# Performance work log

Measured on AMD Instinct MI355X. Metric: run time of the kernel, lower is better.

The kernel has to match this reference:

```python
import jax, jax.numpy as jnp
import numpy as np

N_NODES = 100000
N_EDGES = 640000
LATDIM = 128
GNN_LAYER = 3
LN_EPS = 1e-5


def setup_inputs() -> dict:
    key = jax.random.key(0)
    k1, k2, k3, k4 = jax.random.split(key, 4)
    embeds = jax.random.normal(k1, (N_NODES, LATDIM), dtype=jnp.float32)
    adj_row = jax.random.randint(k2, (N_EDGES,), 0, N_NODES, dtype=jnp.int32)
    adj_col = jax.random.randint(k3, (N_EDGES,), 0, N_NODES, dtype=jnp.int32)
    adj_val = jax.random.uniform(k4, (N_EDGES,), dtype=jnp.float32)
    return {"embeds": embeds, "adj_row": adj_row, "adj_col": adj_col, "adj_val": adj_val}


def _layer_norm(x):
    # nn.LayerNorm(latdim, elementwise_affine=False)
    mu = jnp.mean(x, axis=-1, keepdims=True)
    var = jnp.mean(jnp.square(x - mu), axis=-1, keepdims=True)
    return (x - mu) / jnp.sqrt(var + LN_EPS)


def _spmm(adj_row, adj_col, adj_val, x):
    # out[r] += val * x[c] for each edge (r, c, val)  -- sparse [N,N] @ [N,d]
    msgs = adj_val[:, None] * x[adj_col]  # [E, d]
    return jax.ops.segment_sum(msgs, adj_row, num_segments=N_NODES)


def reference(embeds, adj_row, adj_col, adj_val):
    x = _layer_norm(embeds)
    acc = jnp.zeros_like(x)  # gnn_layer > 0, so hop-0 embeds are NOT included
    for _ in range(GNN_LAYER):
        x = _spmm(adj_row, adj_col, adj_val, x)
        acc = acc + x
    return acc
```

## Files before the change

kernel.cpp:

```cpp
#include <hip/hip_runtime.h>

#define N_NODES 100000
#define N_EDGES 640000
#define LATDIM  128
#define LN_EPS  1e-5f

typedef unsigned int u32;
typedef float f32x4 __attribute__((ext_vector_type(4)));

#define SCAN_NB   98
#define N_PAD     (SCAN_NB * 1024)

#define LN_BLOCKS   (N_NODES / 8)
#define HIST_BLOCKS ((N_EDGES + 255) / 256)

__device__ __forceinline__ float bflo(u32 u) { return __uint_as_float(u << 16); }
__device__ __forceinline__ float bfhi(u32 u) { return __uint_as_float(u & 0xffff0000u); }
__device__ __forceinline__ u32 pack_bf2(float a, float b) {
    u32 ua = __float_as_uint(a), ub = __float_as_uint(b);
    ua = (ua + 0x7fffu + ((ua >> 16) & 1u)) >> 16;
    ub = (ub + 0x7fffu + ((ub >> 16) & 1u)) >> 16;
    return ua | (ub << 16);
}

__device__ __forceinline__ u32 pack_edge(int col, float val) {
    u32 q = (u32)fminf(val * 32768.0f + 0.5f, 32767.0f);
    return (u32)col | (q << 17);
}
__device__ __forceinline__ int   edge_col(u32 r) { return (int)(r & 0x1FFFFu); }
__device__ __forceinline__ float edge_val(u32 r) { return (float)(r >> 17) * (1.0f / 32768.0f); }

__global__ __launch_bounds__(256) void ln_hist_kernel(const float* __restrict__ in,
                                                      u32* __restrict__ out,
                                                      const int* __restrict__ rowi,
                                                      int* __restrict__ cnt) {
    int b = blockIdx.x;
    if (b < LN_BLOCKS) {
        int tid  = threadIdx.x;
        int wave = tid >> 6;
        int lane = tid & 63;
        int half = lane >> 5;
        int sub  = lane & 31;
        int row  = b * 8 + wave * 2 + half;
        f32x4 v = __builtin_nontemporal_load(((const f32x4*)in) + (size_t)row * 32 + sub);
        float s  = v.x + v.y + v.z + v.w;
        float ss = v.x * v.x + v.y * v.y + v.z * v.z + v.w * v.w;
        #pragma unroll
        for (int o = 16; o > 0; o >>= 1) {
            s  += __shfl_xor(s,  o, 64);
            ss += __shfl_xor(ss, o, 64);
        }
        float mu   = s * (1.0f / LATDIM);
        float var  = ss * (1.0f / LATDIM) - mu * mu;
        float rstd = rsqrtf(var + LN_EPS);
        uint2 w;
        w.x = pack_bf2((v.x - mu) * rstd, (v.y - mu) * rstd);
        w.y = pack_bf2((v.z - mu) * rstd, (v.w - mu) * rstd);
        ((uint2*)out)[(size_t)row * 32 + sub] = w;
    } else {
        int e = (b - LN_BLOCKS) * 256 + threadIdx.x;
        if (e < N_EDGES) atomicAdd(&cnt[rowi[e]], 1);
    }
}

__global__ __launch_bounds__(256) void scan_ab_kernel(int* __restrict__ cnt,
                                                      int* __restrict__ bsums,
                                                      int* __restrict__ done) {
    __shared__ int ts[256];
    __shared__ int amLast;
    int t = threadIdx.x;
    int base = blockIdx.x * 1024 + t * 4;
    int4 v = *(const int4*)(cnt + base);
    int s = v.x + v.y + v.z + v.w;
    ts[t] = s;
    __syncthreads();
    #pragma unroll
    for (int o = 1; o < 256; o <<= 1) {
        int u = 0;
        if (t >= o) u = ts[t - o];
        __syncthreads();
        if (t >= o) ts[t] += u;
        __syncthreads();
    }
    int excl = ts[t] - s;
    int4 w;
    w.x = excl;
    w.y = excl + v.x;
    w.z = excl + v.x + v.y;
    w.w = excl + v.x + v.y + v.z;
    *(int4*)(cnt + base) = w;
    if (t == 255) {
        __hip_atomic_store(&bsums[blockIdx.x], ts[255],
                           __ATOMIC_RELEASE, __HIP_MEMORY_SCOPE_AGENT);
        int prev = __hip_atomic_fetch_add(done, 1,
                                          __ATOMIC_ACQ_REL, __HIP_MEMORY_SCOPE_AGENT);
        amLast = (prev == SCAN_NB - 1);
    }
    __syncthreads();
    if (amLast) {
        __shared__ int ss[128];
        int own = 0;
        if (t < 128) {
            own = (t < SCAN_NB)
                ? __hip_atomic_load(&bsums[t], __ATOMIC_ACQUIRE, __HIP_MEMORY_SCOPE_AGENT)
                : 0;
            ss[t] = own;
        }
        __syncthreads();
        #pragma unroll
        for (int o = 1; o < 128; o <<= 1) {
            int u = 0;
            if (t >= o && t < 128) u = ss[t - o];
            __syncthreads();
            if (t >= o && t < 128) ss[t] += u;
            __syncthreads();
        }
        if (t < SCAN_NB) bsums[t] = ss[t] - own;
    }
}

__global__ __launch_bounds__(256) void scatter_kernel(const int* __restrict__ rowi,
                                                      const int* __restrict__ coli,
                                                      const float* __restrict__ vali,
                                                      int* __restrict__ cursor,
                                                      const int* __restrict__ bsums,
                                                      u32* __restrict__ recs) {
    int e = blockIdx.x * 256 + threadIdx.x;
    if (e >= N_EDGES) return;
    int r = rowi[e];
    int pos = atomicAdd(&cursor[r], 1) + bsums[r >> 10];
    recs[pos] = pack_edge(coli[e], vali[e]);
}

__global__ __launch_bounds__(256) void spmm_csr_kernel(const int* __restrict__ row_end,
                                                       const int* __restrict__ bsums,
                                                       const u32* __restrict__ recs,
                                                       const u32* __restrict__ x,
                                                       u32* __restrict__ y,
                                                       const u32* __restrict__ add0,
                                                       const u32* __restrict__ add1,
                                                       float* __restrict__ out,
                                                       int mode) {
    int tid  = threadIdx.x;
    int wave = tid >> 6;
    int lane = tid & 63;
    int row  = blockIdx.x * 16 + wave * 4 + (lane >> 4);
    int sub  = lane & 15;
    int end = row_end[row] + bsums[row >> 10];
    int e   = row ? row_end[row - 1] + bsums[(row - 1) >> 10] : 0;
    const uint4* x4 = (const uint4*)x;
    float a0=0,a1=0,a2=0,a3=0,a4=0,a5=0,a6=0,a7=0;
    for (; e + 4 <= end; e += 4) {
        u32 r0 = recs[e], r1 = recs[e+1], r2 = recs[e+2], r3 = recs[e+3];
        uint4 g0 = x4[(size_t)edge_col(r0) * 16 + sub];
        uint4 g1 = x4[(size_t)edge_col(r1) * 16 + sub];
        uint4 g2 = x4[(size_t)edge_col(r2) * 16 + sub];
        uint4 g3 = x4[(size_t)edge_col(r3) * 16 + sub];
        float v0 = edge_val(r0), v1 = edge_val(r1);
        float v2 = edge_val(r2), v3 = edge_val(r3);
        a0 += v0 * bflo(g0.x); a1 += v0 * bfhi(g0.x);
        a2 += v0 * bflo(g0.y); a3 += v0 * bfhi(g0.y);
        a4 += v0 * bflo(g0.z); a5 += v0 * bfhi(g0.z);
        a6 += v0 * bflo(g0.w); a7 += v0 * bfhi(g0.w);
        a0 += v1 * bflo(g1.x); a1 += v1 * bfhi(g1.x);
        a2 += v1 * bflo(g1.y); a3 += v1 * bfhi(g1.y);
        a4 += v1 * bflo(g1.z); a5 += v1 * bfhi(g1.z);
        a6 += v1 * bflo(g1.w); a7 += v1 * bfhi(g1.w);
        a0 += v2 * bflo(g2.x); a1 += v2 * bfhi(g2.x);
        a2 += v2 * bflo(g2.y); a3 += v2 * bfhi(g2.y);
        a4 += v2 * bflo(g2.z); a5 += v2 * bfhi(g2.z);
        a6 += v2 * bflo(g2.w); a7 += v2 * bfhi(g2.w);
        a0 += v3 * bflo(g3.x); a1 += v3 * bfhi(g3.x);
        a2 += v3 * bflo(g3.y); a3 += v3 * bfhi(g3.y);
        a4 += v3 * bflo(g3.z); a5 += v3 * bfhi(g3.z);
        a6 += v3 * bflo(g3.w); a7 += v3 * bfhi(g3.w);
    }
    for (; e < end; ++e) {
        u32 r = recs[e];
        uint4 g = x4[(size_t)edge_col(r) * 16 + sub];
        float v = edge_val(r);
        a0 += v * bflo(g.x); a1 += v * bfhi(g.x);
        a2 += v * bflo(g.y); a3 += v * bfhi(g.y);
        a4 += v * bflo(g.z); a5 += v * bfhi(g.z);
        a6 += v * bflo(g.w); a7 += v * bfhi(g.w);
    }
    size_t oi = (size_t)row * 16 + sub;
    if (mode == 2) {
        uint4 b0 = ((const uint4*)add0)[oi];
        uint4 b1 = ((const uint4*)add1)[oi];
        a0 += bflo(b0.x) + bflo(b1.x); a1 += bfhi(b0.x) + bfhi(b1.x);
        a2 += bflo(b0.y) + bflo(b1.y); a3 += bfhi(b0.y) + bfhi(b1.y);
        a4 += bflo(b0.z) + bflo(b1.z); a5 += bfhi(b0.z) + bfhi(b1.z);
        a6 += bflo(b0.w) + bflo(b1.w); a7 += bfhi(b0.w) + bfhi(b1.w);
        f32x4* o4 = (f32x4*)(out + (size_t)row * LATDIM + sub * 8);
        f32x4 q0 = {a0, a1, a2, a3};
        f32x4 q1 = {a4, a5, a6, a7};
        __builtin_nontemporal_store(q0, o4 + 0);
        __builtin_nontemporal_store(q1, o4 + 1);
    } else {
        uint4 w;
        w.x = pack_bf2(a0, a1);
        w.y = pack_bf2(a2, a3);
        w.z = pack_bf2(a4, a5);
        w.w = pack_bf2(a6, a7);
        ((uint4*)y)[oi] = w;
    }
}

__global__ __launch_bounds__(256) void ln_f32_kernel(const float* __restrict__ in,
                                                     float* __restrict__ out) {
    int tid  = threadIdx.x;
    int wave = tid >> 6;
    int lane = tid & 63;
    int half = lane >> 5;
    int sub  = lane & 31;
    int row  = blockIdx.x * 8 + wave * 2 + half;
    if (row >= N_NODES) return;
    float4 v = ((const float4*)in)[(size_t)row * 32 + sub];
    float s  = v.x + v.y + v.z + v.w;
    float ss = v.x * v.x + v.y * v.y + v.z * v.z + v.w * v.w;
    #pragma unroll
    for (int o = 16; o > 0; o >>= 1) {
        s  += __shfl_xor(s,  o, 64);
        ss += __shfl_xor(ss, o, 64);
    }
    float mu   = s * (1.0f / LATDIM);
    float var  = ss * (1.0f / LATDIM) - mu * mu;
    float rstd = rsqrtf(var + LN_EPS);
    float4 o4;
    o4.x = (v.x - mu) * rstd; o4.y = (v.y - mu) * rstd;
    o4.z = (v.z - mu) * rstd; o4.w = (v.w - mu) * rstd;
    ((float4*)out)[(size_t)row * 32 + sub] = o4;
}

__global__ __launch_bounds__(256) void spmm_atomic_kernel(const int* __restrict__ rowi,
                                                          const int* __restrict__ coli,
                                                          const float* __restrict__ vali,
                                                          const float* __restrict__ x,
                                                          float* __restrict__ y) {
    int t = blockIdx.x * 256 + threadIdx.x;
    int e = t >> 5;
    if (e >= N_EDGES) return;
    int k = t & 31;
    int r = rowi[e];
    int c = coli[e];
    float v = vali[e];
    float4 xv = ((const float4*)(x + (size_t)c * LATDIM))[k];
    float* yp = y + (size_t)r * LATDIM + k * 4;
    atomicAdd(yp + 0, v * xv.x);
    atomicAdd(yp + 1, v * xv.y);
    atomicAdd(yp + 2, v * xv.z);
    atomicAdd(yp + 3, v * xv.w);
}

__global__ __launch_bounds__(256) void addz_kernel(float* __restrict__ acc,
                                                   const float* __restrict__ x,
                                                   float* __restrict__ z,
                                                   int first) {
    size_t i = (size_t)blockIdx.x * 256 + threadIdx.x;
    float4 xv = ((const float4*)x)[i];
    float4* ap = ((float4*)acc) + i;
    if (first) {
        *ap = xv;
    } else {
        float4 a = *ap;
        a.x += xv.x; a.y += xv.y; a.z += xv.z; a.w += xv.w;
        *ap = a;
    }
    if (z) ((float4*)z)[i] = make_float4(0.f, 0.f, 0.f, 0.f);
}

extern "C" void kernel_launch(void* const* d_in, const int* in_sizes, int n_in,
                              void* d_out, int out_size, void* d_ws, size_t ws_size,
                              hipStream_t stream) {
    const float* embeds  = (const float*)d_in[0];
    const int*   adj_row = (const int*)d_in[1];
    const int*   adj_col = (const int*)d_in[2];
    const float* adj_val = (const float*)d_in[3];
    float* out = (float*)d_out;

    u32*  A16  = (u32*)d_ws;
    u32*  B16  = A16 + (size_t)N_NODES * (LATDIM / 2);
    int*  cnt   = (int*)(B16 + (size_t)N_NODES * (LATDIM / 2));
    int*  bsums = cnt + N_PAD;
    int*  done  = bsums + 128;
    u32*  recs  = (u32*)(done + 32);
    size_t need = (size_t)((char*)(recs + N_EDGES) - (char*)d_ws);

    const int edgeGrid = (N_EDGES + 255) / 256;
    const int rowGrid  = N_NODES / 16;

    if (ws_size >= need) {
        hipMemsetAsync(cnt, 0, (size_t)(N_PAD + 128 + 32) * sizeof(int), stream);
        ln_hist_kernel<<<LN_BLOCKS + HIST_BLOCKS, 256, 0, stream>>>(embeds, A16,
                                                                    adj_row, cnt);
        scan_ab_kernel<<<SCAN_NB, 256, 0, stream>>>(cnt, bsums, done);
        scatter_kernel<<<edgeGrid, 256, 0, stream>>>(adj_row, adj_col, adj_val,
                                                     cnt, bsums, recs);
        spmm_csr_kernel<<<rowGrid, 256, 0, stream>>>(cnt, bsums, recs, A16, B16,
                                                     nullptr, nullptr, nullptr, 0);
        spmm_csr_kernel<<<rowGrid, 256, 0, stream>>>(cnt, bsums, recs, B16, A16,
                                                     nullptr, nullptr, nullptr, 0);
        spmm_csr_kernel<<<rowGrid, 256, 0, stream>>>(cnt, bsums, recs, A16, nullptr,
                                                     B16, A16, out, 2);
    } else {
        float* A = (float*)d_ws;
        float* B = A + (size_t)N_NODES * LATDIM;
        const size_t rowBytes = (size_t)N_NODES * LATDIM * sizeof(float);
        const int spmmGrid = (N_EDGES * 32 + 255) / 256;
        const int addGrid  = (N_NODES * LATDIM / 4 + 255) / 256;
        ln_f32_kernel<<<LN_BLOCKS, 256, 0, stream>>>(embeds, A);
        hipMemsetAsync(B, 0, rowBytes, stream);
        spmm_atomic_kernel<<<spmmGrid, 256, 0, stream>>>(adj_row, adj_col, adj_val, A, B);
        addz_kernel<<<addGrid, 256, 0, stream>>>(out, B, A, 1);
        spmm_atomic_kernel<<<spmmGrid, 256, 0, stream>>>(adj_row, adj_col, adj_val, B, A);
        addz_kernel<<<addGrid, 256, 0, stream>>>(out, A, B, 0);
        spmm_atomic_kernel<<<spmmGrid, 256, 0, stream>>>(adj_row, adj_col, adj_val, A, B);
        addz_kernel<<<addGrid, 256, 0, stream>>>(out, B, nullptr, 0);
    }
}
```

Measured before the change: 267.7 us.

## Replace global-atomic CSR scatter with two-pass bucketed scatter via shared-memory cursors

The old per-edge scatter did one global atomicAdd per edge on row cursors. It is replaced with a coarse pass that bins edges into 1024-row buckets, using a block-local histogram and one global atomic per bucket per block, followed by a fine pass that places edges within each bucket using shared-memory cursors. The fused scan with a last-block atomic is split into two kernels. The change adds a staging buffer of 8 bytes per edge plus two extra kernel launches. The fine pass runs only 98 blocks, which may underuse the GPU.

Measured after the change: 257.0 us. 4.0% less time.

```diff
diff --git a/kernel.cpp b/kernel.cpp
--- a/kernel.cpp
+++ b/kernel.cpp
@@ -13,6 +13,10 @@
 
 #define LN_BLOCKS   (N_NODES / 8)
 #define HIST_BLOCKS ((N_EDGES + 255) / 256)
+
+#define APP_K      7
+#define APP_EDGES  (256 * APP_K)
+#define APP_NB     ((N_EDGES + APP_EDGES - 1) / APP_EDGES)
 
 __device__ __forceinline__ float bflo(u32 u) { return __uint_as_float(u << 16); }
 __device__ __forceinline__ float bfhi(u32 u) { return __uint_as_float(u & 0xffff0000u); }
@@ -63,11 +67,9 @@
     }
 }
 
-__global__ __launch_bounds__(256) void scan_ab_kernel(int* __restrict__ cnt,
-                                                      int* __restrict__ bsums,
-                                                      int* __restrict__ done) {
+__global__ __launch_bounds__(256) void scan_a_kernel(int* __restrict__ cnt,
+                                                     int* __restrict__ csums) {
     __shared__ int ts[256];
-    __shared__ int amLast;
     int t = threadIdx.x;
     int base = blockIdx.x * 1024 + t * 4;
     int4 v = *(const int4*)(cnt + base);
@@ -89,50 +91,94 @@
     w.z = excl + v.x + v.y;
     w.w = excl + v.x + v.y + v.z;
     *(int4*)(cnt + base) = w;
-    if (t == 255) {
-        __hip_atomic_store(&bsums[blockIdx.x], ts[255],
-                           __ATOMIC_RELEASE, __HIP_MEMORY_SCOPE_AGENT);
-        int prev = __hip_atomic_fetch_add(done, 1,
-                                          __ATOMIC_ACQ_REL, __HIP_MEMORY_SCOPE_AGENT);
-        amLast = (prev == SCAN_NB - 1);
-    }
-    __syncthreads();
-    if (amLast) {
-        __shared__ int ss[128];
-        int own = 0;
-        if (t < 128) {
-            own = (t < SCAN_NB)
-                ? __hip_atomic_load(&bsums[t], __ATOMIC_ACQUIRE, __HIP_MEMORY_SCOPE_AGENT)
-                : 0;
-            ss[t] = own;
+    if (t == 255) csums[blockIdx.x] = ts[255];
+}
+
+__global__ __launch_bounds__(128) void scan_b_kernel(const int* __restrict__ csums,
+                                                     int* __restrict__ bsums,
+                                                     int* __restrict__ gcur) {
+    __shared__ int ss[128];
+    int t = threadIdx.x;
+    int own = (t < SCAN_NB) ? csums[t] : 0;
+    ss[t] = own;
+    __syncthreads();
+    #pragma unroll
+    for (int o = 1; o < 128; o <<= 1) {
+        int u = 0;
+        if (t >= o) u = ss[t - o];
+        __syncthreads();
+        if (t >= o) ss[t] += u;
+        __syncthreads();
+    }
+    if (t < SCAN_NB) {
+        int off = ss[t] - own;
+        bsums[t] = off;
+        gcur[t]  = off;
+    }
+    if (t == SCAN_NB) bsums[SCAN_NB] = N_EDGES;
+}
+
+__global__ __launch_bounds__(256) void bucket_append_kernel(const int* __restrict__ rowi,
+                                                            const int* __restrict__ coli,
+                                                            const float* __restrict__ vali,
+                                                            int* __restrict__ gcur,
+                                                            uint2* __restrict__ staging) {
+    __shared__ int hist[SCAN_NB];
+    __shared__ int base[SCAN_NB];
+    int t = threadIdx.x;
+    if (t < SCAN_NB) hist[t] = 0;
+    __syncthreads();
+    int e0 = blockIdx.x * APP_EDGES;
+    int r[APP_K]; int c[APP_K]; float v[APP_K]; int bk[APP_K];
+    #pragma unroll
+    for (int k = 0; k < APP_K; ++k) {
+        int e = e0 + k * 256 + t;
+        if (e < N_EDGES) {
+            r[k] = rowi[e]; c[k] = coli[e]; v[k] = vali[e];
+            bk[k] = r[k] >> 10;
+            atomicAdd(&hist[bk[k]], 1);
+        } else {
+            bk[k] = -1;
         }
-        __syncthreads();
-        #pragma unroll
-        for (int o = 1; o < 128; o <<= 1) {
-            int u = 0;
-            if (t >= o && t < 128) u = ss[t - o];
-            __syncthreads();
-            if (t >= o && t < 128) ss[t] += u;
-            __syncthreads();
+    }
+    __syncthreads();
+    if (t < SCAN_NB) {
+        int h = hist[t];
+        base[t] = h ? atomicAdd(&gcur[t], h) : 0;
+        hist[t] = 0;
+    }
+    __syncthreads();
+    #pragma unroll
+    for (int k = 0; k < APP_K; ++k) {
+        if (bk[k] >= 0) {
+            int idx = atomicAdd(&hist[bk[k]], 1);
+            staging[base[bk[k]] + idx] =
+                make_uint2(((u32)(r[k] & 1023) << 17) | (u32)c[k],
+                           __float_as_uint(v[k]));
         }
-        if (t < SCAN_NB) bsums[t] = ss[t] - own;
-    }
-}
-
-__global__ __launch_bounds__(256) void scatter_kernel(const int* __restrict__ rowi,
-                                                      const int* __restrict__ coli,
-                                                      const float* __restrict__ vali,
-                                                      int* __restrict__ cursor,
-                                                      const int* __restrict__ bsums,
-                                                      u32* __restrict__ recs) {
-    int e = blockIdx.x * 256 + threadIdx.x;
-    if (e >= N_EDGES) return;
-    int r = rowi[e];
-    int pos = atomicAdd(&cursor[r], 1) + bsums[r >> 10];
-    recs[pos] = pack_edge(coli[e], vali[e]);
-}
-
-__global__ __launch_bounds__(256) void spmm_csr_kernel(const int* __restrict__ row_end,
+    }
+}
+
+__global__ __launch_bounds__(256) void fine_scatter_kernel(const int* __restrict__ cnt,
+                                                           const int* __restrict__ bsums,
+                                                           const uint2* __restrict__ staging,
+                                                           u32* __restrict__ recs) {
+    __shared__ int cur[1024];
+    int b = blockIdx.x, t = threadIdx.x;
+    *(int4*)&cur[t * 4] = *(const int4*)&cnt[b * 1024 + t * 4];
+    __syncthreads();
+    int gbase = bsums[b];
+    int n = bsums[b + 1] - gbase;
+    for (int i = t; i < n; i += 256) {
+        uint2 s = staging[gbase + i];
+        int rowLocal = (int)(s.x >> 17);
+        int col = (int)(s.x & 0x1FFFFu);
+        int pos = gbase + atomicAdd(&cur[rowLocal], 1);
+        recs[pos] = pack_edge(col, __uint_as_float(s.y));
+    }
+}
+
+__global__ __launch_bounds__(256) void spmm_csr_kernel(const int* __restrict__ cnt,
                                                        const int* __restrict__ bsums,
                                                        const u32* __restrict__ recs,
                                                        const u32* __restrict__ x,
@@ -146,8 +192,8 @@
     int lane = tid & 63;
     int row  = blockIdx.x * 16 + wave * 4 + (lane >> 4);
     int sub  = lane & 15;
-    int end = row_end[row] + bsums[row >> 10];
-    int e   = row ? row_end[row - 1] + bsums[(row - 1) >> 10] : 0;
+    int e   = cnt[row]     + bsums[row >> 10];
+    int end = cnt[row + 1] + bsums[(row + 1) >> 10];
     const uint4* x4 = (const uint4*)x;
     float a0=0,a1=0,a2=0,a3=0,a4=0,a5=0,a6=0,a7=0;
     for (; e + 4 <= end; e += 4) {
@@ -279,24 +325,27 @@
     const float* adj_val = (const float*)d_in[3];
     float* out = (float*)d_out;
 
-    u32*  A16  = (u32*)d_ws;
-    u32*  B16  = A16 + (size_t)N_NODES * (LATDIM / 2);
-    int*  cnt   = (int*)(B16 + (size_t)N_NODES * (LATDIM / 2));
-    int*  bsums = cnt + N_PAD;
-    int*  done  = bsums + 128;
-    u32*  recs  = (u32*)(done + 32);
-    size_t need = (size_t)((char*)(recs + N_EDGES) - (char*)d_ws);
-
-    const int edgeGrid = (N_EDGES + 255) / 256;
-    const int rowGrid  = N_NODES / 16;
+    u32*   A16   = (u32*)d_ws;
+    u32*   B16   = A16 + (size_t)N_NODES * (LATDIM / 2);
+    int*   cnt   = (int*)(B16 + (size_t)N_NODES * (LATDIM / 2));
+    int*   csums = cnt + N_PAD;
+    int*   bsums = csums + 128;
+    int*   gcur  = bsums + 128;
+    uint2* staging = (uint2*)(gcur + 128);
+    u32*   recs  = (u32*)(staging + N_EDGES);
+    size_t need  = (size_t)((char*)(recs + N_EDGES) - (char*)d_ws);
+
+    const int rowGrid = N_NODES / 16;
 
     if (ws_size >= need) {
-        hipMemsetAsync(cnt, 0, (size_t)(N_PAD + 128 + 32) * sizeof(int), stream);
+        hipMemsetAsync(cnt, 0, (size_t)N_PAD * sizeof(int), stream);
         ln_hist_kernel<<<LN_BLOCKS + HIST_BLOCKS, 256, 0, stream>>>(embeds, A16,
                                                                     adj_row, cnt);
-        scan_ab_kernel<<<SCAN_NB, 256, 0, stream>>>(cnt, bsums, done);
-        scatter_kernel<<<edgeGrid, 256, 0, stream>>>(adj_row, adj_col, adj_val,
-                                                     cnt, bsums, recs);
+        scan_a_kernel<<<SCAN_NB, 256, 0, stream>>>(cnt, csums);
+        scan_b_kernel<<<1, 128, 0, stream>>>(csums, bsums, gcur);
+        bucket_append_kernel<<<APP_NB, 256, 0, stream>>>(adj_row, adj_col, adj_val,
+                                                         gcur, staging);
+        fine_scatter_kernel<<<SCAN_NB, 256, 0, stream>>>(cnt, bsums, staging, recs);
         spmm_csr_kernel<<<rowGrid, 256, 0, stream>>>(cnt, bsums, recs, A16, B16,
                                                      nullptr, nullptr, nullptr, 0);
         spmm_csr_kernel<<<rowGrid, 256, 0, stream>>>(cnt, bsums, recs, B16, A16,
```
